# Kernel optimization log

Hardware: AMD Instinct MI355X
Metric: run time of the kernel (lower is better)

The kernel has to match this reference:

```python
import jax, jax.numpy as jnp
import numpy as np
import math

B, N, C = 8, 1024, 256
NUM_HEAD = 4
HEAD_DIM = C // NUM_HEAD
K_NN = 5
SAMPLE_RATIO = 0.25
CLUSTER_NUM = max(math.ceil(N * SAMPLE_RATIO), 1)
EPS = 1e-6


def cluster_dpc_knn(x, cluster_num, k):
    # DPC-KNN clustering (faithful to TCFormer's cluster_dpc_knn, run under no_grad in torch)
    b, n, c = x.shape
    sq = jnp.sum(x * x, axis=-1)
    d2 = sq[:, :, None] + sq[:, None, :] - 2.0 * jnp.einsum('bic,bjc->bij', x, x)
    dist = jnp.sqrt(jnp.maximum(d2, 0.0)) / jnp.sqrt(jnp.asarray(c, x.dtype))  # (b,n,n)
    # k smallest distances per token (includes self, dist 0)
    neg_near, _ = jax.lax.top_k(-dist, k)
    dist_nearest = -neg_near
    density = jnp.exp(-jnp.mean(dist_nearest ** 2, axis=-1))  # (b,n)
    # deterministic tiny noise for tie-breaking (torch adds rand*1e-6)
    density = density + jax.random.uniform(jax.random.key(42), density.shape, dtype=density.dtype) * 1e-6
    mask = (density[:, None, :] > density[:, :, None]).astype(x.dtype)
    dist_max = jnp.max(dist.reshape(b, -1), axis=-1)[:, None, None]
    d_ind = jnp.min(dist * mask + dist_max * (1.0 - mask), axis=-1)  # distance indicator
    score = d_ind * density
    _, index_down = jax.lax.top_k(score, cluster_num)  # (b,cluster_num) cluster centers
    dist_c = jnp.take_along_axis(dist, index_down[:, :, None], axis=1)  # (b,cn,n)
    idx_cluster = jnp.argmin(dist_c, axis=1)  # (b,n)
    # ensure each center maps to its own cluster id
    bidx = jnp.arange(b)[:, None]
    idx_cluster = idx_cluster.at[bidx, index_down].set(jnp.broadcast_to(jnp.arange(cluster_num)[None, :], (b, cluster_num)))
    return idx_cluster


def setup_inputs() -> dict:
    key = jax.random.key(0)
    ks = jax.random.split(key, 6)
    w_scale = 1.0 / jnp.sqrt(jnp.asarray(C, jnp.float32))
    x_token = jax.random.normal(ks[0], (B, N, C), dtype=jnp.float32)
    Wq = jax.random.normal(ks[1], (C, C), dtype=jnp.float32) * w_scale
    Wk = jax.random.normal(ks[2], (C, C), dtype=jnp.float32) * w_scale
    Wv = jax.random.normal(ks[3], (C, C), dtype=jnp.float32) * w_scale
    Wp = jax.random.normal(ks[4], (C, C), dtype=jnp.float32) * w_scale
    bp = jax.random.normal(ks[5], (C,), dtype=jnp.float32) * 0.01
    return {"x_token": x_token, "Wq": Wq, "Wk": Wk, "Wv": Wv, "Wp": Wp, "bp": bp}


def reference(x_token, Wq, Wk, Wv, Wp, bp):
    b, n, c = x_token.shape
    scale = HEAD_DIM ** -0.5
    idx_cluster = cluster_dpc_knn(x_token, CLUSTER_NUM, K_NN)  # (b,n) int
    q = (x_token @ Wq.T).reshape(b, n, NUM_HEAD, HEAD_DIM).transpose(0, 2, 1, 3)
    k = (x_token @ Wk.T).reshape(b, n, NUM_HEAD, HEAD_DIM).transpose(0, 2, 1, 3)
    v = (x_token @ Wv.T).reshape(b, n, NUM_HEAD, HEAD_DIM).transpose(0, 2, 1, 3)
    scores = jnp.einsum('bhid,bhjd->bhij', q, k) * scale  # (b,h,n,n)
    # scatter into (b,cluster_num,n,c) + sum over clusters == mask scores by same-cluster
    same = (idx_cluster[:, :, None] == idx_cluster[:, None, :])[:, None, :, :]
    attn = jnp.where(same, scores, 0.0)
    # original: masked_fill(attn == 0, -1e9) then exp in float32
    attn = jnp.where(attn == 0.0, -1e9, attn)
    attn = jnp.exp(attn.astype(jnp.float32))
    attn = (attn + EPS / n) / (jnp.sum(attn, axis=-1, keepdims=True) + EPS)
    out = jnp.einsum('bhij,bhjd->bhid', attn, v).transpose(0, 2, 1, 3).reshape(b, n, c)
    return out @ Wp.T + bp
```

## Files before the change

### kernel.cpp

```cpp
#include <hip/hip_runtime.h>
#include <math.h>

#define B_ 8
#define N_ 1024
#define C_ 256
#define H_ 4
#define D_ 64
#define CN_ 256
#define EPS_ 1e-6f

__device__ __forceinline__ unsigned rotl32(unsigned x, int r){ return (x<<r)|(x>>(32-r)); }

__device__ float tf_noise(unsigned gid){
  unsigned c0 = (gid >= 4096u) ? gid - 4096u : gid;
  unsigned c1 = c0 + 4096u;
  const unsigned k0 = 0u, k1 = 42u;
  const unsigned ks2 = k0 ^ k1 ^ 0x1BD11BDAu;
  unsigned x0 = c0 + k0, x1 = c1 + k1;
  const int R0[4] = {13,15,26,6};
  const int R1[4] = {17,29,16,24};
  #pragma unroll
  for (int i=0;i<4;i++){ x0 += x1; x1 = rotl32(x1,R0[i]); x1 ^= x0; }
  x0 += k1; x1 += ks2 + 1u;
  #pragma unroll
  for (int i=0;i<4;i++){ x0 += x1; x1 = rotl32(x1,R1[i]); x1 ^= x0; }
  x0 += ks2; x1 += k0 + 2u;
  #pragma unroll
  for (int i=0;i<4;i++){ x0 += x1; x1 = rotl32(x1,R0[i]); x1 ^= x0; }
  x0 += k0; x1 += k1 + 3u;
  #pragma unroll
  for (int i=0;i<4;i++){ x0 += x1; x1 = rotl32(x1,R1[i]); x1 ^= x0; }
  x0 += k1; x1 += ks2 + 4u;
  #pragma unroll
  for (int i=0;i<4;i++){ x0 += x1; x1 = rotl32(x1,R0[i]); x1 ^= x0; }
  x0 += ks2; x1 += k0 + 5u;
  unsigned bits = (gid >= 4096u) ? x1 : x0;
  return __uint_as_float(0x3F800000u | (bits >> 9)) - 1.0f;
}

__global__ __launch_bounds__(256) void k_sq(const float* __restrict__ x, float* __restrict__ sq){
  int row = blockIdx.x * 4 + (threadIdx.x >> 6);
  int l = threadIdx.x & 63;
  const float* p = x + (size_t)row * C_;
  float s = 0.f;
  #pragma unroll
  for (int t=0;t<4;t++){ float v = p[l + 64*t]; s += v*v; }
  #pragma unroll
  for (int m=32;m;m>>=1) s += __shfl_xor(s, m);
  if (l==0) sq[row] = s;
}

__global__ __launch_bounds__(256) void k_dist4(const float* __restrict__ x, const float* __restrict__ sq,
                                               float* __restrict__ dist){
  int b = blockIdx.z, bi = blockIdx.y, bj = blockIdx.x;
  const float* xb = x + (size_t)b*N_*C_;
  const float* pa = xb + (size_t)(bi*128)*C_;
  const float* pb = xb + (size_t)(bj*128)*C_;
  __shared__ float As[32][132];
  __shared__ float Bs[32][132];
  int tid = threadIdx.x;
  int tx = tid & 15, ty = tid >> 4;
  float acc[8][8] = {};
  for (int k0=0;k0<C_;k0+=32){
    #pragma unroll
    for (int f=0; f<4; f++){
      int e = f*256 + tid; int row = e>>3, kq = e&7;
      float4 a = *(const float4*)(pa + (size_t)row*C_ + k0 + kq*4);
      float4 c = *(const float4*)(pb + (size_t)row*C_ + k0 + kq*4);
      As[kq*4+0][row]=a.x; As[kq*4+1][row]=a.y; As[kq*4+2][row]=a.z; As[kq*4+3][row]=a.w;
      Bs[kq*4+0][row]=c.x; Bs[kq*4+1][row]=c.y; Bs[kq*4+2][row]=c.z; Bs[kq*4+3][row]=c.w;
    }
    __syncthreads();
    #pragma unroll
    for (int kk=0;kk<32;kk++){
      float4 a0 = *(const float4*)&As[kk][ty*4];
      float4 a1 = *(const float4*)&As[kk][64+ty*4];
      float4 b0 = *(const float4*)&Bs[kk][tx*4];
      float4 b1 = *(const float4*)&Bs[kk][64+tx*4];
      float av[8]={a0.x,a0.y,a0.z,a0.w,a1.x,a1.y,a1.z,a1.w};
      float bv[8]={b0.x,b0.y,b0.z,b0.w,b1.x,b1.y,b1.z,b1.w};
      #pragma unroll
      for (int r=0;r<8;r++)
        #pragma unroll
        for (int c=0;c<8;c++) acc[r][c] += av[r]*bv[c];
    }
    __syncthreads();
  }
  float sqj[8];
  #pragma unroll
  for (int cc=0;cc<2;cc++)
    #pragma unroll
    for (int c=0;c<4;c++) sqj[cc*4+c] = sq[b*N_ + bj*128 + cc*64 + tx*4 + c];
  float* dbase = dist + (size_t)b*N_*N_;
  #pragma unroll
  for (int rr=0;rr<2;rr++){
    #pragma unroll
    for (int r=0;r<4;r++){
      int i = bi*128 + rr*64 + ty*4 + r;
      float si = sq[b*N_ + i];
      #pragma unroll
      for (int cc=0;cc<2;cc++){
        int j0 = bj*128 + cc*64 + tx*4;
        float o[4];
        #pragma unroll
        for (int c=0;c<4;c++){
          float d2 = si + sqj[cc*4+c] - 2.f*acc[rr*4+r][cc*4+c];
          o[c] = sqrtf(fmaxf(d2, 0.f)) * 0.0625f;
        }
        *(float4*)(dbase + (size_t)i*N_ + j0) = make_float4(o[0],o[1],o[2],o[3]);
      }
    }
  }
}

__global__ __launch_bounds__(256) void k_proj(const float* __restrict__ X,
    const float* __restrict__ W0, const float* __restrict__ W1, const float* __restrict__ W2,
    const float* __restrict__ bias,
    float* __restrict__ Y0, float* __restrict__ Y1, float* __restrict__ Y2){
  const float* W = (blockIdx.z==0)?W0:(blockIdx.z==1)?W1:W2;
  float* Y = (blockIdx.z==0)?Y0:(blockIdx.z==1)?Y1:Y2;
  int bi = blockIdx.y, bj = blockIdx.x;
  const float* pa = X + (size_t)(bi*128)*C_;
  const float* pb = W + (size_t)(bj*64)*C_;
  __shared__ float As[32][132];
  __shared__ float Bs[32][68];
  int tid = threadIdx.x;
  int tx = tid & 15, ty = tid >> 4;
  float acc[8][4] = {};
  for (int k0=0;k0<C_;k0+=32){
    #pragma unroll
    for (int f=0; f<4; f++){
      int e = f*256 + tid; int row = e>>3, kq = e&7;
      float4 a = *(const float4*)(pa + (size_t)row*C_ + k0 + kq*4);
      As[kq*4+0][row]=a.x; As[kq*4+1][row]=a.y; As[kq*4+2][row]=a.z; As[kq*4+3][row]=a.w;
    }
    #pragma unroll
    for (int f=0; f<2; f++){
      int e = f*256 + tid; int row = e>>3, kq = e&7;
      float4 c = *(const float4*)(pb + (size_t)row*C_ + k0 + kq*4);
      Bs[kq*4+0][row]=c.x; Bs[kq*4+1][row]=c.y; Bs[kq*4+2][row]=c.z; Bs[kq*4+3][row]=c.w;
    }
    __syncthreads();
    #pragma unroll
    for (int kk=0;kk<32;kk++){
      float4 a0 = *(const float4*)&As[kk][ty*4];
      float4 a1 = *(const float4*)&As[kk][64+ty*4];
      float4 b0 = *(const float4*)&Bs[kk][tx*4];
      float av[8]={a0.x,a0.y,a0.z,a0.w,a1.x,a1.y,a1.z,a1.w};
      float bv[4]={b0.x,b0.y,b0.z,b0.w};
      #pragma unroll
      for (int r=0;r<8;r++)
        #pragma unroll
        for (int c=0;c<4;c++) acc[r][c] += av[r]*bv[c];
    }
    __syncthreads();
  }
  float bs[4];
  #pragma unroll
  for (int c=0;c<4;c++) bs[c] = bias ? bias[bj*64 + tx*4 + c] : 0.f;
  #pragma unroll
  for (int rr=0;rr<2;rr++)
    #pragma unroll
    for (int r=0;r<4;r++){
      int m = bi*128 + rr*64 + ty*4 + r;
      int j0 = bj*64 + tx*4;
      *(float4*)(Y + (size_t)m*C_ + j0) =
        make_float4(acc[rr*4+r][0]+bs[0], acc[rr*4+r][1]+bs[1],
                    acc[rr*4+r][2]+bs[2], acc[rr*4+r][3]+bs[3]);
    }
}

__global__ __launch_bounds__(256) void k_top5(const float* __restrict__ dist, float* __restrict__ density,
                                              float* __restrict__ rowmax){
  int row = blockIdx.x * 4 + (threadIdx.x >> 6);
  int l = threadIdx.x & 63;
  const float* p = dist + (size_t)row * N_;
  float t[5] = {1e30f,1e30f,1e30f,1e30f,1e30f};
  float mx = 0.f;
  #pragma unroll
  for (int q2=0;q2<16;q2++){
    float v = p[l + 64*q2];
    mx = fmaxf(mx, v);
    if (v < t[4]){
      t[4] = v;
      #pragma unroll
      for (int a=4;a>0;a--) if (t[a] < t[a-1]) { float tmp=t[a]; t[a]=t[a-1]; t[a-1]=tmp; }
    }
  }
  #pragma unroll
  for (int m=32;m;m>>=1) mx = fmaxf(mx, __shfl_xor(mx, m));
  float sumsq = 0.f;
  int hi = 0;
  #pragma unroll
  for (int a=0;a<5;a++){
    float head = (hi==0)?t[0]:(hi==1)?t[1]:(hi==2)?t[2]:(hi==3)?t[3]:(hi==4)?t[4]:1e30f;
    float m = head;
    #pragma unroll
    for (int mm=32;mm;mm>>=1) m = fminf(m, __shfl_xor(m, mm));
    sumsq += m*m;
    unsigned long long ball = __ballot(head == m);
    if (l == (__ffsll(ball) - 1)) hi++;
  }
  if (l == 0){
    float msq = sumsq / 5.0f;
    density[row] = expf(-msq) + tf_noise((unsigned)row) * 1e-6f;
    rowmax[row] = mx;
  }
}

__global__ __launch_bounds__(256) void k_bmax(const float* __restrict__ rowmax, float* __restrict__ bmax){
  int b = blockIdx.x; int t = threadIdx.x;
  float m = fmaxf(fmaxf(rowmax[b*N_+t], rowmax[b*N_+t+256]),
                  fmaxf(rowmax[b*N_+t+512], rowmax[b*N_+t+768]));
  __shared__ float s[256];
  s[t]=m; __syncthreads();
  for (int d=128; d; d>>=1){ if (t<d) s[t]=fmaxf(s[t],s[t+d]); __syncthreads(); }
  if (t==0) bmax[b]=s[0];
}

__global__ __launch_bounds__(256) void k_dind(const float* __restrict__ dist, const float* __restrict__ density,
                                              const float* __restrict__ bmax, float* __restrict__ score){
  int row = blockIdx.x * 4 + (threadIdx.x >> 6);
  int b = row >> 10;
  int l = threadIdx.x & 63;
  const float* p = dist + (size_t)row * N_;
  const float* db = density + b*N_;
  float di = density[row];
  float m = bmax[b];
  #pragma unroll
  for (int q2=0;q2<16;q2++){
    int j = l + 64*q2;
    float dj = db[j];
    if (dj > di) m = fminf(m, p[j]);
  }
  #pragma unroll
  for (int mm=32;mm;mm>>=1) m = fminf(m, __shfl_xor(m, mm));
  if (l==0) score[row] = m * di;
}

__global__ __launch_bounds__(1024) void k_top256(const float* __restrict__ score, int* __restrict__ idxdown){
  int b = blockIdx.x; int t = threadIdx.x;
  __shared__ float sv[1024];
  __shared__ int si[1024];
  float v = score[b*N_ + t];
  int i = t;
  for (int k = 2; k <= 1024; k <<= 1){
    for (int j = k >> 1; j > 0; j >>= 1){
      float v2; int i2;
      if (j >= 64){
        sv[t] = v; si[t] = i;
        __syncthreads();
        v2 = sv[t ^ j]; i2 = si[t ^ j];
        __syncthreads();
      } else {
        v2 = __shfl_xor(v, j);
        i2 = __shfl_xor(i, j);
      }
      bool islo = (t & j) == 0;
      float lov = islo ? v : v2,  hiv = islo ? v2 : v;
      int   loi = islo ? i : i2,  hii = islo ? i2 : i;
      bool prec = (lov > hiv) || (lov == hiv && loi < hii);
      bool up = ((t & k) == 0);
      bool dosw = up ? !prec : prec;
      if (dosw){ v = v2; i = i2; }
    }
  }
  if (t < CN_) idxdown[b*CN_ + t] = i;
}

__global__ __launch_bounds__(256) void k_assign(const float* __restrict__ dist, const int* __restrict__ idxdown,
                                                int* __restrict__ idxclu){
  int b = blockIdx.y;
  int l = threadIdx.x & 63;
  int ch = threadIdx.x >> 6;
  int j = blockIdx.x*64 + l;
  __shared__ int cen[256];
  __shared__ float sd[4][64];
  __shared__ int sk[4][64];
  cen[threadIdx.x] = idxdown[b*CN_ + threadIdx.x];
  __syncthreads();
  const float* dbase = dist + (size_t)b*N_*N_;
  float best = 1e30f; int bk = 0;
  #pragma unroll 8
  for (int kk=0; kk<64; kk++){
    int k = ch*64 + kk;
    float d = dbase[(size_t)cen[k]*N_ + j];
    if (d < best){ best = d; bk = k; }
  }
  sd[ch][l] = best; sk[ch][l] = bk;
  __syncthreads();
  if (ch == 0){
    #pragma unroll
    for (int c2=1;c2<4;c2++){
      float d = sd[c2][l];
      if (d < best){ best = d; bk = sk[c2][l]; }
    }
    idxclu[b*N_ + j] = bk;
  }
}

__global__ void k_setcenters(const int* __restrict__ idxdown, int* __restrict__ idxclu){
  int b = blockIdx.x; int t = threadIdx.x;
  idxclu[b*N_ + idxdown[b*CN_ + t]] = t;
}

__global__ __launch_bounds__(256) void k_build(const int* __restrict__ idxclu, int* __restrict__ off,
                                               int* __restrict__ cnt, int* __restrict__ members){
  int b = blockIdx.x; int t = threadIdx.x;
  __shared__ int sc[256], so[256];
  sc[t] = 0;
  __syncthreads();
  int cl[4];
  #pragma unroll
  for (int i=0;i<4;i++){
    cl[i] = idxclu[b*N_ + i*256 + t];
    atomicAdd(&sc[cl[i]], 1);
  }
  __syncthreads();
  int mine = sc[t];
  so[t] = mine;
  __syncthreads();
  for (int d=1; d<256; d<<=1){
    int v2 = 0;
    if (t>=d) v2 = so[t-d];
    __syncthreads();
    if (t>=d) so[t] += v2;
    __syncthreads();
  }
  int excl = so[t] - mine;
  off[b*CN_+t] = excl;
  cnt[b*CN_+t] = mine;
  sc[t] = excl;
  __syncthreads();
  #pragma unroll
  for (int i=0;i<4;i++){
    int p = atomicAdd(&sc[cl[i]], 1);
    members[b*N_ + p] = i*256 + t;
  }
}

__global__ __launch_bounds__(256) void k_vsum1(const float* __restrict__ v, float* __restrict__ vsp){
  int p = blockIdx.x;
  int b = p >> 4, s = p & 15;
  int c = threadIdx.x;
  float acc = 0.f;
  const float* base = v + ((size_t)b*N_ + s*64)*C_ + c;
  #pragma unroll 8
  for (int i=0;i<64;i++) acc += base[(size_t)i*C_];
  vsp[(size_t)p*C_ + c] = acc;
}

__global__ __launch_bounds__(256) void k_vsum2(const float* __restrict__ vsp, float* __restrict__ vsum){
  int b = blockIdx.x; int c = threadIdx.x;
  float s = 0.f;
  #pragma unroll
  for (int i=0;i<16;i++) s += vsp[((size_t)b*16 + i)*C_ + c];
  vsum[b*C_ + c] = s;
}

__global__ __launch_bounds__(256) void k_attn(const float* __restrict__ q, const float* __restrict__ kmat,
                                              const float* __restrict__ v, const float* __restrict__ vsum,
                                              const int* __restrict__ idxclu, const int* __restrict__ off,
                                              const int* __restrict__ cnt, const int* __restrict__ members,
                                              float* __restrict__ att){
  int bi = blockIdx.x;
  int b = bi >> 10;
  int h = threadIdx.x >> 6, l = threadIdx.x & 63;
  int c = idxclu[bi];
  int o = off[b*CN_ + c], m = cnt[b*CN_ + c];
  int ch = h*64 + l;
  float qv = q[(size_t)bi*C_ + ch];
  float acc = 0.f, den = 0.f;
  const int* mem = members + b*N_ + o;
  for (int t=0;t<m;t++){
    int j = mem[t];
    size_t base = ((size_t)(b*N_ + j))*C_ + ch;
    float p = qv * kmat[base];
    #pragma unroll
    for (int mm=32;mm;mm>>=1) p += __shfl_xor(p, mm);
    float s = p * 0.125f;
    float e = (s == 0.0f) ? 0.0f : expf(s);
    den += e;
    acc += e * v[base];
  }
  float outv = (acc + (EPS_/1024.0f) * vsum[b*C_ + ch]) / (den + EPS_);
  att[(size_t)bi*C_ + ch] = outv;
}

extern "C" void kernel_launch(void* const* d_in, const int* in_sizes, int n_in,
                              void* d_out, int out_size, void* d_ws, size_t ws_size,
                              hipStream_t stream){
  const float* x  = (const float*)d_in[0];
  const float* Wq = (const float*)d_in[1];
  const float* Wk = (const float*)d_in[2];
  const float* Wv = (const float*)d_in[3];
  const float* Wp = (const float*)d_in[4];
  const float* bp = (const float*)d_in[5];
  float* out = (float*)d_out;

  float* ws = (float*)d_ws;
  float* dist    = ws;
  float* q       = dist + (size_t)B_*N_*N_;
  float* kk      = q    + (size_t)B_*N_*C_;
  float* v       = kk   + (size_t)B_*N_*C_;
  float* att     = v    + (size_t)B_*N_*C_;
  float* vsp     = att  + (size_t)B_*N_*C_;
  float* vsum    = vsp + 128*C_;
  float* sq      = vsum + B_*C_;
  float* rowmax  = sq + B_*N_;
  float* bmax    = rowmax + B_*N_;
  float* density = bmax + 16;
  float* score   = density + B_*N_;
  int* idxdown   = (int*)(score + B_*N_);
  int* idxclu    = idxdown + B_*CN_;
  int* cnt       = idxclu + B_*N_;
  int* off       = cnt + B_*CN_;
  int* members   = off + B_*CN_;

  k_sq<<<B_*N_/4,256,0,stream>>>(x, sq);
  k_dist4<<<dim3(8,8,8),256,0,stream>>>(x, sq, dist);
  k_top5<<<B_*N_/4,256,0,stream>>>(dist, density, rowmax);
  k_bmax<<<8,256,0,stream>>>(rowmax, bmax);
  k_dind<<<B_*N_/4,256,0,stream>>>(dist, density, bmax, score);
  k_top256<<<8,1024,0,stream>>>(score, idxdown);
  k_assign<<<dim3(16,8),256,0,stream>>>(dist, idxdown, idxclu);
  k_setcenters<<<8,256,0,stream>>>(idxdown, idxclu);
  k_build<<<8,256,0,stream>>>(idxclu, off, cnt, members);
  k_proj<<<dim3(4,64,3),256,0,stream>>>(x, Wq, Wk, Wv, nullptr, q, kk, v);
  k_vsum1<<<128,256,0,stream>>>(v, vsp);
  k_vsum2<<<8,256,0,stream>>>(vsp, vsum);
  k_attn<<<B_*N_,256,0,stream>>>(q, kk, v, vsum, idxclu, off, cnt, members, att);
  k_proj<<<dim3(4,64,1),256,0,stream>>>(att, Wp, Wp, Wp, bp, out, out, out);
}
```

Before: 302.7 us.

## Pre-transpose activations and weights so GEMM tiles stage with contiguous float4 copies

Adds transpose kernels that write x, the attention output and the four weight matrices into K-major layouts. The distance and projection GEMMs can then copy tiles into shared memory with direct float4 stores instead of scattered transposing stores. The distance kernel moves to 128x64 tiles with more blocks, and the center-setting kernel is merged into the cluster-build kernel. This adds extra transpose passes and launches, and reuses the dist and att buffers as scratch for the transposed data.

```diff
diff --git a/kernel.cpp b/kernel.cpp
--- a/kernel.cpp
+++ b/kernel.cpp
@@ -4,8 +4,6 @@
 #define B_ 8
 #define N_ 1024
 #define C_ 256
-#define H_ 4
-#define D_ 64
 #define CN_ 256
 #define EPS_ 1e-6f
 
@@ -50,109 +48,136 @@
   if (l==0) sq[row] = s;
 }
 
-__global__ __launch_bounds__(256) void k_dist4(const float* __restrict__ x, const float* __restrict__ sq,
+__global__ __launch_bounds__(256) void k_trx(const float* __restrict__ src, float* __restrict__ dst){
+  int z = blockIdx.z, rb = blockIdx.y*64, cb = blockIdx.x*64;
+  const float* s = src + (size_t)z*N_*C_;
+  float* d = dst + (size_t)z*N_*C_;
+  __shared__ float t[64][65];
+  int tid = threadIdx.x;
+  int hr = tid>>4, c4 = (tid&15)*4;
+  #pragma unroll
+  for (int p=0;p<4;p++){
+    int r = p*16 + hr;
+    float4 v = *(const float4*)(s + (size_t)(rb+r)*C_ + cb + c4);
+    t[r][c4+0]=v.x; t[r][c4+1]=v.y; t[r][c4+2]=v.z; t[r][c4+3]=v.w;
+  }
+  __syncthreads();
+  int r4 = (tid&15)*4;
+  #pragma unroll
+  for (int p=0;p<4;p++){
+    int c = p*16 + hr;
+    *(float4*)(d + (size_t)(cb+c)*N_ + rb + r4) =
+      make_float4(t[r4+0][c], t[r4+1][c], t[r4+2][c], t[r4+3][c]);
+  }
+}
+
+__global__ __launch_bounds__(256) void k_trw(const float* __restrict__ s0, const float* __restrict__ s1,
+                                             const float* __restrict__ s2, const float* __restrict__ s3,
+                                             float* __restrict__ dst){
+  int z = blockIdx.z;
+  const float* s = (z==0)?s0:(z==1)?s1:(z==2)?s2:s3;
+  float* d = dst + (size_t)z*C_*C_;
+  int rb = blockIdx.y*64, cb = blockIdx.x*64;
+  __shared__ float t[64][65];
+  int tid = threadIdx.x;
+  int hr = tid>>4, c4 = (tid&15)*4;
+  #pragma unroll
+  for (int p=0;p<4;p++){
+    int r = p*16 + hr;
+    float4 v = *(const float4*)(s + (size_t)(rb+r)*C_ + cb + c4);
+    t[r][c4+0]=v.x; t[r][c4+1]=v.y; t[r][c4+2]=v.z; t[r][c4+3]=v.w;
+  }
+  __syncthreads();
+  int r4 = (tid&15)*4;
+  #pragma unroll
+  for (int p=0;p<4;p++){
+    int c = p*16 + hr;
+    *(float4*)(d + (size_t)(cb+c)*C_ + rb + r4) =
+      make_float4(t[r4+0][c], t[r4+1][c], t[r4+2][c], t[r4+3][c]);
+  }
+}
+
+#define STAGE_A(SRC, LDA)                                                      \
+  _Pragma("unroll")                                                            \
+  for (int rno=0;rno<4;rno++){                                                 \
+    int l = rno*1024 + tid*4; int k = l>>7, n = l&127;                         \
+    *(float4*)&As[l] = *(const float4*)((SRC) + (size_t)(k0+k)*(LDA) + n);     \
+  }
+#define STAGE_B(SRC, LDB)                                                      \
+  _Pragma("unroll")                                                            \
+  for (int rno=0;rno<2;rno++){                                                 \
+    int l = rno*1024 + tid*4; int k = l>>6, j = l&63;                          \
+    *(float4*)&Bs[l] = *(const float4*)((SRC) + (size_t)(k0+k)*(LDB) + j);     \
+  }
+#define INNER84                                                                \
+  _Pragma("unroll")                                                            \
+  for (int kk=0;kk<32;kk++){                                                   \
+    float4 a0 = *(const float4*)&As[kk*128 + ty*4];                            \
+    float4 a1 = *(const float4*)&As[kk*128 + 64 + ty*4];                       \
+    float4 b0 = *(const float4*)&Bs[kk*64 + tx*4];                             \
+    float av[8]={a0.x,a0.y,a0.z,a0.w,a1.x,a1.y,a1.z,a1.w};                     \
+    float bv[4]={b0.x,b0.y,b0.z,b0.w};                                         \
+    _Pragma("unroll")                                                          \
+    for (int r=0;r<8;r++)                                                      \
+      _Pragma("unroll")                                                        \
+      for (int c=0;c<4;c++) acc[r][c] += av[r]*bv[c];                          \
+  }
+
+__global__ __launch_bounds__(256) void k_dist5(const float* __restrict__ xT, const float* __restrict__ sq,
                                                float* __restrict__ dist){
   int b = blockIdx.z, bi = blockIdx.y, bj = blockIdx.x;
-  const float* xb = x + (size_t)b*N_*C_;
-  const float* pa = xb + (size_t)(bi*128)*C_;
-  const float* pb = xb + (size_t)(bj*128)*C_;
-  __shared__ float As[32][132];
-  __shared__ float Bs[32][132];
-  int tid = threadIdx.x;
-  int tx = tid & 15, ty = tid >> 4;
-  float acc[8][8] = {};
+  const float* At = xT + (size_t)b*C_*N_ + bi*128;
+  const float* Bt = xT + (size_t)b*C_*N_ + bj*64;
+  __shared__ float As[32*128];
+  __shared__ float Bs[32*64];
+  int tid = threadIdx.x, tx = tid&15, ty = tid>>4;
+  float acc[8][4] = {};
   for (int k0=0;k0<C_;k0+=32){
-    #pragma unroll
-    for (int f=0; f<4; f++){
-      int e = f*256 + tid; int row = e>>3, kq = e&7;
-      float4 a = *(const float4*)(pa + (size_t)row*C_ + k0 + kq*4);
-      float4 c = *(const float4*)(pb + (size_t)row*C_ + k0 + kq*4);
-      As[kq*4+0][row]=a.x; As[kq*4+1][row]=a.y; As[kq*4+2][row]=a.z; As[kq*4+3][row]=a.w;
-      Bs[kq*4+0][row]=c.x; Bs[kq*4+1][row]=c.y; Bs[kq*4+2][row]=c.z; Bs[kq*4+3][row]=c.w;
-    }
-    __syncthreads();
-    #pragma unroll
-    for (int kk=0;kk<32;kk++){
-      float4 a0 = *(const float4*)&As[kk][ty*4];
-      float4 a1 = *(const float4*)&As[kk][64+ty*4];
-      float4 b0 = *(const float4*)&Bs[kk][tx*4];
-      float4 b1 = *(const float4*)&Bs[kk][64+tx*4];
-      float av[8]={a0.x,a0.y,a0.z,a0.w,a1.x,a1.y,a1.z,a1.w};
-      float bv[8]={b0.x,b0.y,b0.z,b0.w,b1.x,b1.y,b1.z,b1.w};
-      #pragma unroll
-      for (int r=0;r<8;r++)
-        #pragma unroll
-        for (int c=0;c<8;c++) acc[r][c] += av[r]*bv[c];
-    }
-    __syncthreads();
-  }
-  float sqj[8];
-  #pragma unroll
-  for (int cc=0;cc<2;cc++)
-    #pragma unroll
-    for (int c=0;c<4;c++) sqj[cc*4+c] = sq[b*N_ + bj*128 + cc*64 + tx*4 + c];
+    STAGE_A(At, N_)
+    STAGE_B(Bt, N_)
+    __syncthreads();
+    INNER84
+    __syncthreads();
+  }
+  float sqj[4];
+  #pragma unroll
+  for (int c=0;c<4;c++) sqj[c] = sq[b*N_ + bj*64 + tx*4 + c];
   float* dbase = dist + (size_t)b*N_*N_;
   #pragma unroll
-  for (int rr=0;rr<2;rr++){
+  for (int rr=0;rr<2;rr++)
     #pragma unroll
     for (int r=0;r<4;r++){
       int i = bi*128 + rr*64 + ty*4 + r;
       float si = sq[b*N_ + i];
+      float o[4];
       #pragma unroll
-      for (int cc=0;cc<2;cc++){
-        int j0 = bj*128 + cc*64 + tx*4;
-        float o[4];
-        #pragma unroll
-        for (int c=0;c<4;c++){
-          float d2 = si + sqj[cc*4+c] - 2.f*acc[rr*4+r][cc*4+c];
-          o[c] = sqrtf(fmaxf(d2, 0.f)) * 0.0625f;
-        }
-        *(float4*)(dbase + (size_t)i*N_ + j0) = make_float4(o[0],o[1],o[2],o[3]);
+      for (int c=0;c<4;c++){
+        float d2 = si + sqj[c] - 2.f*acc[rr*4+r][c];
+        o[c] = sqrtf(fmaxf(d2, 0.f)) * 0.0625f;
       }
+      *(float4*)(dbase + (size_t)i*N_ + bj*64 + tx*4) = make_float4(o[0],o[1],o[2],o[3]);
     }
-  }
-}
-
-__global__ __launch_bounds__(256) void k_proj(const float* __restrict__ X,
-    const float* __restrict__ W0, const float* __restrict__ W1, const float* __restrict__ W2,
+}
+
+__global__ __launch_bounds__(256) void k_proj5(const float* __restrict__ AT,
+    const float* __restrict__ BT0, const float* __restrict__ BT1, const float* __restrict__ BT2,
     const float* __restrict__ bias,
     float* __restrict__ Y0, float* __restrict__ Y1, float* __restrict__ Y2){
-  const float* W = (blockIdx.z==0)?W0:(blockIdx.z==1)?W1:W2;
+  const float* BT = (blockIdx.z==0)?BT0:(blockIdx.z==1)?BT1:BT2;
   float* Y = (blockIdx.z==0)?Y0:(blockIdx.z==1)?Y1:Y2;
   int bi = blockIdx.y, bj = blockIdx.x;
-  const float* pa = X + (size_t)(bi*128)*C_;
-  const float* pb = W + (size_t)(bj*64)*C_;
-  __shared__ float As[32][132];
-  __shared__ float Bs[32][68];
-  int tid = threadIdx.x;
-  int tx = tid & 15, ty = tid >> 4;
+  int bb = bi>>3, n0 = (bi&7)*128;
+  const float* At = AT + (size_t)bb*C_*N_ + n0;
+  const float* Bt = BT + bj*64;
+  __shared__ float As[32*128];
+  __shared__ float Bs[32*64];
+  int tid = threadIdx.x, tx = tid&15, ty = tid>>4;
   float acc[8][4] = {};
   for (int k0=0;k0<C_;k0+=32){
-    #pragma unroll
-    for (int f=0; f<4; f++){
-      int e = f*256 + tid; int row = e>>3, kq = e&7;
-      float4 a = *(const float4*)(pa + (size_t)row*C_ + k0 + kq*4);
-      As[kq*4+0][row]=a.x; As[kq*4+1][row]=a.y; As[kq*4+2][row]=a.z; As[kq*4+3][row]=a.w;
-    }
-    #pragma unroll
-    for (int f=0; f<2; f++){
-      int e = f*256 + tid; int row = e>>3, kq = e&7;
-      float4 c = *(const float4*)(pb + (size_t)row*C_ + k0 + kq*4);
-      Bs[kq*4+0][row]=c.x; Bs[kq*4+1][row]=c.y; Bs[kq*4+2][row]=c.z; Bs[kq*4+3][row]=c.w;
-    }
-    __syncthreads();
-    #pragma unroll
-    for (int kk=0;kk<32;kk++){
-      float4 a0 = *(const float4*)&As[kk][ty*4];
-      float4 a1 = *(const float4*)&As[kk][64+ty*4];
-      float4 b0 = *(const float4*)&Bs[kk][tx*4];
-      float av[8]={a0.x,a0.y,a0.z,a0.w,a1.x,a1.y,a1.z,a1.w};
-      float bv[4]={b0.x,b0.y,b0.z,b0.w};
-      #pragma unroll
-      for (int r=0;r<8;r++)
-        #pragma unroll
-        for (int c=0;c<4;c++) acc[r][c] += av[r]*bv[c];
-    }
+    STAGE_A(At, N_)
+    STAGE_B(Bt, C_)
+    __syncthreads();
+    INNER84
     __syncthreads();
   }
   float bs[4];
@@ -163,8 +188,7 @@
     #pragma unroll
     for (int r=0;r<4;r++){
       int m = bi*128 + rr*64 + ty*4 + r;
-      int j0 = bj*64 + tx*4;
-      *(float4*)(Y + (size_t)m*C_ + j0) =
+      *(float4*)(Y + (size_t)m*C_ + bj*64 + tx*4) =
         make_float4(acc[rr*4+r][0]+bs[0], acc[rr*4+r][1]+bs[1],
                     acc[rr*4+r][2]+bs[2], acc[rr*4+r][3]+bs[3]);
     }
@@ -299,14 +323,12 @@
   }
 }
 
-__global__ void k_setcenters(const int* __restrict__ idxdown, int* __restrict__ idxclu){
+__global__ __launch_bounds__(256) void k_build2(const int* __restrict__ idxdown, int* __restrict__ idxclu,
+                                                int* __restrict__ off, int* __restrict__ cnt,
+                                                int* __restrict__ members){
   int b = blockIdx.x; int t = threadIdx.x;
   idxclu[b*N_ + idxdown[b*CN_ + t]] = t;
-}
-
-__global__ __launch_bounds__(256) void k_build(const int* __restrict__ idxclu, int* __restrict__ off,
-                                               int* __restrict__ cnt, int* __restrict__ members){
-  int b = blockIdx.x; int t = threadIdx.x;
+  __syncthreads();
   __shared__ int sc[256], so[256];
   sc[t] = 0;
   __syncthreads();
@@ -404,7 +426,8 @@
   float* kk      = q    + (size_t)B_*N_*C_;
   float* v       = kk   + (size_t)B_*N_*C_;
   float* att     = v    + (size_t)B_*N_*C_;
-  float* vsp     = att  + (size_t)B_*N_*C_;
+  float* WT      = att  + (size_t)B_*N_*C_;
+  float* vsp     = WT + 4*C_*C_;
   float* vsum    = vsp + 128*C_;
   float* sq      = vsum + B_*C_;
   float* rowmax  = sq + B_*N_;
@@ -417,18 +440,23 @@
   int* off       = cnt + B_*CN_;
   int* members   = off + B_*CN_;
 
+  float* xT   = att;
+  float* attT = dist;
+
+  k_trx<<<dim3(4,16,8),256,0,stream>>>(x, xT);
+  k_trw<<<dim3(4,4,4),256,0,stream>>>(Wq, Wk, Wv, Wp, WT);
   k_sq<<<B_*N_/4,256,0,stream>>>(x, sq);
-  k_dist4<<<dim3(8,8,8),256,0,stream>>>(x, sq, dist);
+  k_dist5<<<dim3(16,8,8),256,0,stream>>>(xT, sq, dist);
   k_top5<<<B_*N_/4,256,0,stream>>>(dist, density, rowmax);
   k_bmax<<<8,256,0,stream>>>(rowmax, bmax);
   k_dind<<<B_*N_/4,256,0,stream>>>(dist, density, bmax, score);
   k_top256<<<8,1024,0,stream>>>(score, idxdown);
   k_assign<<<dim3(16,8),256,0,stream>>>(dist, idxdown, idxclu);
-  k_setcenters<<<8,256,0,stream>>>(idxdown, idxclu);
-  k_build<<<8,256,0,stream>>>(idxclu, off, cnt, members);
-  k_proj<<<dim3(4,64,3),256,0,stream>>>(x, Wq, Wk, Wv, nullptr, q, kk, v);
+  k_build2<<<8,256,0,stream>>>(idxdown, idxclu, off, cnt, members);
+  k_proj5<<<dim3(4,64,3),256,0,stream>>>(xT, WT, WT + C_*C_, WT + 2*C_*C_, nullptr, q, kk, v);
   k_vsum1<<<128,256,0,stream>>>(v, vsp);
   k_vsum2<<<8,256,0,stream>>>(vsp, vsum);
   k_attn<<<B_*N_,256,0,stream>>>(q, kk, v, vsum, idxclu, off, cnt, members, att);
-  k_proj<<<dim3(4,64,1),256,0,stream>>>(att, Wp, Wp, Wp, bp, out, out, out);
-}
+  k_trx<<<dim3(4,16,8),256,0,stream>>>(att, attT);
+  k_proj5<<<dim3(4,64,1),256,0,stream>>>(attT, WT + 3*C_*C_, WT + 3*C_*C_, WT + 3*C_*C_, bp, out, out, out);
+}
```

After: 309.4 us. +2.2%, slower.
